# Optimization experiments

Measured on AMD Instinct MI355X. Metric: run time of the kernel, lower is better.

## Reference

```python
import jax, jax.numpy as jnp
import numpy as np


def setup_inputs() -> dict:
    key = jax.random.key(0)
    ks = jax.random.split(key, 12)
    B, C, H, W = 8, 256, 64, 64
    inter = C // 8
    s = 0.05  # weight scale keeps q.k logits in a stable softmax range
    f32 = jnp.float32
    x = jax.random.normal(ks[0], (B, C, H, W), f32)
    Wq = jax.random.normal(ks[1], (inter, C), f32) * s
    bq = jnp.zeros((inter,), f32)
    Wk = jax.random.normal(ks[2], (inter, C), f32) * s
    bk = jnp.zeros((inter,), f32)
    Wv = jax.random.normal(ks[3], (C, C), f32) * s
    bv = jnp.zeros((C,), f32)
    gamma = jnp.full((1,), 0.5, f32)  # learnable residual scale (init 0 in torch; 0.5 exercises the path)
    Wg1 = jax.random.normal(ks[4], (inter, C), f32) * s
    bg1 = jnp.zeros((inter,), f32)
    Wg2 = jax.random.normal(ks[5], (C, inter), f32) * s
    bg2 = jnp.zeros((C,), f32)
    return {"x": x, "Wq": Wq, "bq": bq, "Wk": Wk, "bk": bk, "Wv": Wv, "bv": bv,
            "gamma": gamma, "Wg1": Wg1, "bg1": bg1, "Wg2": Wg2, "bg2": bg2}


def reference(x, Wq, bq, Wk, bk, Wv, bv, gamma, Wg1, bg1, Wg2, bg2):
    B, C, H, W = x.shape
    N = H * W
    xf = x.reshape(B, C, N)  # [B,C,N]
    # 1x1 convs == per-pixel linear projections
    q = jnp.einsum('oc,bcn->bon', Wq, xf) + bq[None, :, None]  # [B,inter,N]
    k = jnp.einsum('oc,bcn->bon', Wk, xf) + bk[None, :, None]  # [B,inter,N]
    v = jnp.einsum('oc,bcn->bon', Wv, xf) + bv[None, :, None]  # [B,C,N]
    # attention[b,n,m] = softmax_m( q[b,:,n] . k[b,:,m] )
    attn = jax.nn.softmax(jnp.einsum('bin,bim->bnm', q, k), axis=-1)  # [B,N,N]
    # out[b,c,n] = sum_m v[b,c,m] * attn[b,n,m]
    out = jnp.einsum('bcm,bnm->bcn', v, attn)  # [B,C,N]
    out = gamma[0] * out + xf
    # gated global pooling branch: GAP -> 1x1 conv -> ReLU -> 1x1 conv -> Sigmoid
    gp = xf.mean(axis=-1)  # [B,C]
    h = jax.nn.relu(jnp.einsum('oc,bc->bo', Wg1, gp) + bg1)  # [B,inter]
    ga = jax.nn.sigmoid(jnp.einsum('co,bo->bc', Wg2, h) + bg2)  # [B,C]
    out = out * ga[:, :, None] + out
    return out.reshape(B, C, H, W)
```

## Files before the change

### kernel.cpp

```cpp
#include <hip/hip_runtime.h>

typedef unsigned short u16;
typedef unsigned int   u32;
typedef short s16x4 __attribute__((ext_vector_type(4)));
typedef u16 u16x4 __attribute__((ext_vector_type(4)));
typedef u16 u16x8 __attribute__((ext_vector_type(8)));
typedef __bf16 bf16x8 __attribute__((ext_vector_type(8)));
typedef float f32x4 __attribute__((ext_vector_type(4)));

#define NB 8
#define NC 256
#define NI 32
#define NN 4096
#define LOG2E 1.4426950408889634f
#define POFF 64.0f

#define OW_Q   0
#define OB_Q   8192
#define OW_K   8224
#define OB_K   16416
#define OW_V   16448
#define OB_V   81984
#define OGAM   82240
#define OW_G1  82248
#define OB_G1  90440
#define OW_G2  90472
#define OB_G2  98664
#define WTOT   98920

__device__ __forceinline__ float bf2f(u16 v) {
    u32 u = ((u32)v) << 16;
    return __builtin_bit_cast(float, u);
}
__device__ __forceinline__ u16 f2bf(float f) {
    u32 u = __builtin_bit_cast(u32, f);
    u32 lsb = (u >> 16) & 1u;
    u += 0x7fffu + lsb;
    return (u16)(u >> 16);
}
__device__ __forceinline__ bool is_f32_mode(const void* graw) {
    return ((const u16*)graw)[0] == 0;
}

__global__ __launch_bounds__(256) void convert_kernel(
    const void* x,  const void* Wq, const void* bq, const void* Wk, const void* bk,
    const void* Wv, const void* bv, const void* gamma, const void* Wg1, const void* bg1,
    const void* Wg2, const void* bg2, float* __restrict__ xf, float* __restrict__ wbuf,
    u16* __restrict__ wbf, float* __restrict__ gp)
{
    bool f32m = is_f32_mode(gamma);
    int blk = blockIdx.x, t = threadIdx.x;
    if (blk < 2048) {
        int base = blk * 4096 + t * 16;
        float s = 0.f;
        if (f32m) {
            const float* xs = (const float*)x;
#pragma unroll
            for (int k = 0; k < 4; ++k) {
                f32x4 a = *(const f32x4*)(xs + base + k * 4);
                s += (a[0] + a[1]) + (a[2] + a[3]);
            }
        } else {
            const u16* xs = (const u16*)x;
#pragma unroll
            for (int k = 0; k < 2; ++k) {
                u16x8 a = *(const u16x8*)(xs + base + k * 8);
                f32x4 lo, hi;
#pragma unroll
                for (int j = 0; j < 4; ++j) { lo[j] = bf2f(a[j]); hi[j] = bf2f(a[4 + j]); }
                *(f32x4*)(xf + base + k * 8)     = lo;
                *(f32x4*)(xf + base + k * 8 + 4) = hi;
                s += (lo[0]+lo[1])+(lo[2]+lo[3]) + (hi[0]+hi[1])+(hi[2]+hi[3]);
            }
        }
#pragma unroll
        for (int off = 1; off <= 32; off <<= 1) s += __shfl_xor(s, off, 64);
        __shared__ float ws[4];
        if ((t & 63) == 0) ws[t >> 6] = s;
        __syncthreads();
        if (t == 0) gp[blk] = (ws[0] + ws[1] + ws[2] + ws[3]) * (1.0f / NN);
        return;
    }
    if (blk < 2080) {
        int tid = (blk - 2048) * 256 + t;
        const int off[12] = {OW_Q, OB_Q, OW_K, OB_K, OW_V, OB_V, OGAM, OW_G1, OB_G1, OW_G2, OB_G2, WTOT};
        const int len[11] = {8192, 32, 8192, 32, 65536, 256, 1, 8192, 32, 8192, 256};
        const void* srcs[11] = {Wq, bq, Wk, bk, Wv, bv, gamma, Wg1, bg1, Wg2, bg2};
        for (int w = tid; w < WTOT; w += 32 * 256) {
            int seg = 0;
#pragma unroll
            for (int i = 1; i < 11; ++i) if (w >= off[i]) seg = i;
            int idx = w - off[seg];
            float val = 0.f;
            if (idx < len[seg])
                val = f32m ? ((const float*)srcs[seg])[idx] : bf2f(((const u16*)srcs[seg])[idx]);
            wbuf[w] = val;
        }
        return;
    }
    int tid = (blk - 2080) * 256 + t;
    for (int w = tid; w < 320 * 256; w += 10 * 256) {
        int row = w >> 8, c = w & 255;
        const void* src; int idx; float scale = 1.f;
        if (row < 32)      { src = Wq; idx = row * 256 + c; scale = LOG2E; }
        else if (row < 64) { src = Wk; idx = (row - 32) * 256 + c; }
        else               { src = Wv; idx = (row - 64) * 256 + c; }
        float val = f32m ? ((const float*)src)[idx] : bf2f(((const u16*)src)[idx]);
        wbf[w] = f2bf(val * scale);
    }
}

__global__ __launch_bounds__(256) void proj_kernel(
    const void* xr, const float* __restrict__ xf, const void* graw,
    const float* __restrict__ wbuf, const u16* __restrict__ wbf,
    u16* __restrict__ qt, u16* __restrict__ kt, u16* __restrict__ v)
{
    __shared__ __attribute__((aligned(16))) u16 xs[64][264];

    const float* X = is_f32_mode(graw) ? (const float*)xr : xf;

    int t    = threadIdx.x;
    int lane = t & 63;
    int wave = t >> 6;
    int b    = blockIdx.x >> 6;
    int m0   = (blockIdx.x & 63) << 6;
    int l15  = lane & 15;
    int quad = lane >> 4;

    {
        const float* xb = X + (size_t)b * NC * NN + m0 + lane;
        int c0 = wave * 64;
#pragma unroll
        for (int ci = 0; ci < 64; ci += 4) {
            int c = c0 + ci;
            float a0 = xb[(size_t)(c    ) * NN];
            float a1 = xb[(size_t)(c + 1) * NN];
            float a2 = xb[(size_t)(c + 2) * NN];
            float a3 = xb[(size_t)(c + 3) * NN];
            u16x4 p4 = { f2bf(a0), f2bf(a1), f2bf(a2), f2bf(a3) };
            *(u16x4*)&xs[lane][c] = p4;
        }
    }
    __syncthreads();

    const f32x4 zero4 = {};
    f32x4 acc[5][4];
#pragma unroll
    for (int i = 0; i < 5; ++i)
#pragma unroll
        for (int mt = 0; mt < 4; ++mt) acc[i][mt] = zero4;

    int obase = wave * 80;
    const u16* wb = wbf + (size_t)(obase + l15) * 256 + quad * 8;

    bf16x8 af[5];
#pragma unroll
    for (int i = 0; i < 5; ++i)
        af[i] = *(const bf16x8*)(wb + (size_t)(i * 16) * 256);

#pragma unroll
    for (int kc = 0; kc < 8; ++kc) {
        bf16x8 afn[5], bfr[4];
        if (kc < 7) {
#pragma unroll
            for (int i = 0; i < 5; ++i)
                afn[i] = *(const bf16x8*)(wb + (size_t)(i * 16) * 256 + (kc + 1) * 32);
        }
#pragma unroll
        for (int mt = 0; mt < 4; ++mt)
            bfr[mt] = *(const bf16x8*)&xs[mt * 16 + l15][kc * 32 + quad * 8];
#pragma unroll
        for (int i = 0; i < 5; ++i)
#pragma unroll
            for (int mt = 0; mt < 4; ++mt)
                acc[i][mt] = __builtin_amdgcn_mfma_f32_16x16x32_bf16(af[i], bfr[mt], acc[i][mt], 0, 0, 0);
        if (kc < 7) {
#pragma unroll
            for (int i = 0; i < 5; ++i) af[i] = afn[i];
        }
    }

    __syncthreads();

    if (wave == 0) {
#pragma unroll
        for (int i = 0; i < 4; ++i) {
#pragma unroll
            for (int mt = 0; mt < 4; ++mt) {
                u16x4 tmp;
#pragma unroll
                for (int r = 0; r < 4; ++r) {
                    int o = i * 16 + quad * 4 + r;
                    float bias = (o < 32) ? LOG2E * wbuf[OB_Q + o] : wbuf[OB_K + o - 32];
                    tmp[r] = f2bf(acc[i][mt][r] + bias);
                }
                *(u16x4*)&xs[mt * 16 + l15][i * 16 + quad * 4] = tmp;
            }
        }
        int m = m0 + lane;
        u16* qrow = qt + (size_t)(b * NN + m) * NI;
        u16* krow = kt + (size_t)(b * NN + m) * NI;
#pragma unroll
        for (int j = 0; j < 4; ++j) *(u16x8*)(qrow + j * 8) = *(const u16x8*)&xs[lane][j * 8];
#pragma unroll
        for (int j = 0; j < 4; ++j) *(u16x8*)(krow + j * 8) = *(const u16x8*)&xs[lane][32 + j * 8];
#pragma unroll
        for (int mt = 0; mt < 4; ++mt) {
#pragma unroll
            for (int r = 0; r < 4; ++r) {
                int c = quad * 4 + r;
                v[(size_t)(b * NC + c) * NN + m0 + mt * 16 + l15] = f2bf(acc[4][mt][r] + wbuf[OB_V + c]);
            }
        }
    } else {
#pragma unroll
        for (int i = 0; i < 5; ++i) {
#pragma unroll
            for (int mt = 0; mt < 4; ++mt) {
#pragma unroll
                for (int r = 0; r < 4; ++r) {
                    int c = wave * 80 + i * 16 + quad * 4 + r - 64;
                    v[(size_t)(b * NC + c) * NN + m0 + mt * 16 + l15] = f2bf(acc[i][mt][r] + wbuf[OB_V + c]);
                }
            }
        }
    }
}

__global__ __launch_bounds__(256) void gate_kernel(
    const float* __restrict__ gp, const float* __restrict__ wbuf, float* __restrict__ gmul)
{
    int b = blockIdx.x;
    int t = threadIdx.x;
    __shared__ float gps[NC];
    __shared__ float hs[NI];
    gps[t] = gp[b * NC + t];
    __syncthreads();
    if (t < NI) {
        float a = wbuf[OB_G1 + t];
        for (int c = 0; c < NC; ++c) a += wbuf[OW_G1 + t * NC + c] * gps[c];
        hs[t] = a > 0.f ? a : 0.f;
    }
    __syncthreads();
    float a = wbuf[OB_G2 + t];
#pragma unroll
    for (int i = 0; i < NI; ++i) a += wbuf[OW_G2 + t * NI + i] * hs[i];
    float sig = 1.f / (1.f + __expf(-a));
    gmul[b * NC + t] = 1.f + sig;
}

__global__ __launch_bounds__(512, 4) void flash_kernel(
    const u16* __restrict__ qt, const u16* __restrict__ kt, const u16* __restrict__ v,
    const void* xr, const float* __restrict__ xf, const void* graw,
    const float* __restrict__ wbuf, const float* __restrict__ gmul, void* outp)
{
    __shared__ __attribute__((aligned(16))) u16 vs[2][NC][48];

    bool f32m = is_f32_mode(graw);
    const float* X = f32m ? (const float*)xr : xf;

    int t    = threadIdx.x;
    int lane = t & 63;
    int wave = t >> 6;
    int b    = blockIdx.x >> 6;
    int nblk = (blockIdx.x & 63) << 6;
    int n0   = nblk + (wave >> 2) * 32;
    int c0   = (wave & 3) * 64;
    int l15  = lane & 15;
    int quad = lane >> 4;

    const f32x4 zero4 = {};

    bf16x8 qf[2];
#pragma unroll
    for (int n16 = 0; n16 < 2; ++n16)
        qf[n16] = *(const bf16x8*)(qt + (size_t)(b * NN + n0 + n16 * 16 + l15) * NI + quad * 8);

    f32x4 acc[2][4];
#pragma unroll
    for (int n16 = 0; n16 < 2; ++n16)
#pragma unroll
        for (int ct = 0; ct < 4; ++ct) acc[n16][ct] = zero4;
    float psum[2] = {0.f, 0.f};

    int sc = t >> 2;
    int sm = (t & 3) * 8;
    const u16* vb0 = v + (size_t)(b * NC + sc) * NN + sm;
    const u16* vb1 = v + (size_t)(b * NC + sc + 128) * NN + sm;
    const u16* ktb = kt + (size_t)(b * NN + l15) * NI + quad * 8;

    u16x8 vr0 = *(const u16x8*)vb0;
    u16x8 vr1 = *(const u16x8*)vb1;
    *(u16x8*)&vs[0][sc][sm]       = vr0;
    *(u16x8*)&vs[0][sc + 128][sm] = vr1;
    bf16x8 ktf[2];
#pragma unroll
    for (int mt = 0; mt < 2; ++mt)
        ktf[mt] = *(const bf16x8*)(ktb + (size_t)(mt * 16) * NI);
    __syncthreads();

    for (int it = 0; it < NN / 32; ++it) {
        int cur  = it & 1;
        bool more = (it < NN / 32 - 1);
        int mnxt = it * 32 + 32;

        if (more) {
            vr0 = *(const u16x8*)(vb0 + mnxt);
            vr1 = *(const u16x8*)(vb1 + mnxt);
        }

        f32x4 sf[2][2];
#pragma unroll
        for (int mt = 0; mt < 2; ++mt)
#pragma unroll
            for (int n16 = 0; n16 < 2; ++n16)
                sf[n16][mt] = __builtin_amdgcn_mfma_f32_16x16x32_bf16(ktf[mt], qf[n16], zero4, 0, 0, 0);

        if (more) {
#pragma unroll
            for (int mt = 0; mt < 2; ++mt)
                ktf[mt] = *(const bf16x8*)(ktb + (size_t)(mnxt + mt * 16) * NI);
        }

        s16x4 pfr[2][2];
#pragma unroll
        for (int n16 = 0; n16 < 2; ++n16)
#pragma unroll
            for (int mt = 0; mt < 2; ++mt) {
                float p0 = __builtin_amdgcn_exp2f(sf[n16][mt][0] - POFF);
                float p1 = __builtin_amdgcn_exp2f(sf[n16][mt][1] - POFF);
                float p2 = __builtin_amdgcn_exp2f(sf[n16][mt][2] - POFF);
                float p3 = __builtin_amdgcn_exp2f(sf[n16][mt][3] - POFF);
                psum[n16] += (p0 + p1) + (p2 + p3);
                pfr[n16][mt] = s16x4{ (short)f2bf(p0), (short)f2bf(p1),
                                      (short)f2bf(p2), (short)f2bf(p3) };
            }

#pragma unroll
        for (int mt = 0; mt < 2; ++mt) {
            int mb = mt * 16 + quad * 4;
#pragma unroll
            for (int ct = 0; ct < 4; ++ct) {
                s16x4 va = *(const s16x4*)&vs[cur][c0 + ct * 16 + l15][mb];
#pragma unroll
                for (int n16 = 0; n16 < 2; ++n16)
                    acc[n16][ct] = __builtin_amdgcn_mfma_f32_16x16x16bf16_1k(va, pfr[n16][mt], acc[n16][ct], 0, 0, 0);
            }
        }

        if (more) {
            *(u16x8*)&vs[cur ^ 1][sc][sm]       = vr0;
            *(u16x8*)&vs[cur ^ 1][sc + 128][sm] = vr1;
        }
        __syncthreads();
    }

    float inv[2];
#pragma unroll
    for (int n16 = 0; n16 < 2; ++n16) {
        float s = psum[n16];
        s += __shfl_xor(s, 16, 64);
        s += __shfl_xor(s, 32, 64);
        inv[n16] = 1.f / s;
    }
    float gam = wbuf[OGAM];

#pragma unroll
    for (int n16 = 0; n16 < 2; ++n16) {
        int n = n0 + n16 * 16 + l15;
#pragma unroll
        for (int ct = 0; ct < 4; ++ct) {
            int cb = c0 + ct * 16 + quad * 4;
            f32x4 gm4 = *(const f32x4*)&gmul[b * NC + cb];
#pragma unroll
            for (int r = 0; r < 4; ++r) {
                size_t off = (size_t)(b * NC + cb + r) * NN + n;
                float val = (gam * acc[n16][ct][r] * inv[n16] + X[off]) * gm4[r];
                if (f32m) ((float*)outp)[off] = val;
                else      ((u16*)outp)[off]  = f2bf(val);
            }
        }
    }
}

extern "C" void kernel_launch(void* const* d_in, const int* in_sizes, int n_in,
                              void* d_out, int out_size, void* d_ws, size_t ws_size,
                              hipStream_t stream)
{
    const void* x     = d_in[0];
    const void* Wq    = d_in[1];
    const void* bq    = d_in[2];
    const void* Wk    = d_in[3];
    const void* bk    = d_in[4];
    const void* Wv    = d_in[5];
    const void* bvp   = d_in[6];
    const void* gamma = d_in[7];
    const void* Wg1   = d_in[8];
    const void* bg1   = d_in[9];
    const void* Wg2   = d_in[10];
    const void* bg2   = d_in[11];

    char* ws = (char*)d_ws;
    float* xf   = (float*)ws;
    float* wbuf = (float*)(ws + 33554432);
    u16*   qt   = (u16*)  (ws + 33951744);
    u16*   kt   = (u16*)  (ws + 36048896);
    u16*   v    = (u16*)  (ws + 38146048);
    float* gp   = (float*)(ws + 54923264);
    float* gmul = (float*)(ws + 54931456);
    u16*   wbf  = (u16*)  (ws + 54939648);

    convert_kernel<<<2090, 256, 0, stream>>>(x, Wq, bq, Wk, bk, Wv, bvp, gamma,
                                             Wg1, bg1, Wg2, bg2, xf, wbuf, wbf, gp);
    proj_kernel<<<NB * 64, 256, 0, stream>>>(x, xf, gamma, wbuf, wbf, qt, kt, v);
    gate_kernel<<<NB, 256, 0, stream>>>(gp, wbuf, gmul);
    flash_kernel<<<NB * 64, 512, 0, stream>>>(qt, kt, v, x, xf, gamma, wbuf, gmul, d_out);
}
```

Baseline: 321.6 us.

## Drop LDS staging of V, read V fragments directly from global memory

Removes the double-buffered shared-memory tile for V and the per-iteration block barrier. Each wave now loads its V MFMA operands straight from global memory (relying on cache) and processes 64 keys per outer step with K prefetch. It also swaps the round-to-nearest bf16 conversion of probabilities for a truncating byte-permute pack. The trade is more global/L2 traffic and latency exposure per wave in exchange for no LDS or sync overhead, plus slightly less accurate bf16 rounding.

```diff
diff --git a/kernel.cpp b/kernel.cpp
--- a/kernel.cpp
+++ b/kernel.cpp
@@ -5,6 +5,7 @@
 typedef short s16x4 __attribute__((ext_vector_type(4)));
 typedef u16 u16x4 __attribute__((ext_vector_type(4)));
 typedef u16 u16x8 __attribute__((ext_vector_type(8)));
+typedef u32 u32x2 __attribute__((ext_vector_type(2)));
 typedef __bf16 bf16x8 __attribute__((ext_vector_type(8)));
 typedef float f32x4 __attribute__((ext_vector_type(4)));
 
@@ -37,6 +38,10 @@
     u32 lsb = (u >> 16) & 1u;
     u += 0x7fffu + lsb;
     return (u16)(u >> 16);
+}
+__device__ __forceinline__ u32 pack_trunc(float f0, float f1) {
+    return __builtin_amdgcn_perm(__builtin_bit_cast(u32, f1),
+                                 __builtin_bit_cast(u32, f0), 0x07060302u);
 }
 __device__ __forceinline__ bool is_f32_mode(const void* graw) {
     return ((const u16*)graw)[0] == 0;
@@ -254,8 +259,6 @@
     const void* xr, const float* __restrict__ xf, const void* graw,
     const float* __restrict__ wbuf, const float* __restrict__ gmul, void* outp)
 {
-    __shared__ __attribute__((aligned(16))) u16 vs[2][NC][48];
-
     bool f32m = is_f32_mode(graw);
     const float* X = f32m ? (const float*)xr : xf;
 
@@ -283,76 +286,63 @@
         for (int ct = 0; ct < 4; ++ct) acc[n16][ct] = zero4;
     float psum[2] = {0.f, 0.f};
 
-    int sc = t >> 2;
-    int sm = (t & 3) * 8;
-    const u16* vb0 = v + (size_t)(b * NC + sc) * NN + sm;
-    const u16* vb1 = v + (size_t)(b * NC + sc + 128) * NN + sm;
     const u16* ktb = kt + (size_t)(b * NN + l15) * NI + quad * 8;
-
-    u16x8 vr0 = *(const u16x8*)vb0;
-    u16x8 vr1 = *(const u16x8*)vb1;
-    *(u16x8*)&vs[0][sc][sm]       = vr0;
-    *(u16x8*)&vs[0][sc + 128][sm] = vr1;
-    bf16x8 ktf[2];
-#pragma unroll
-    for (int mt = 0; mt < 2; ++mt)
+    const u16* vfb = v + (size_t)(b * NC + c0 + l15) * NN + quad * 4;
+
+    bf16x8 ktf[4];
+#pragma unroll
+    for (int mt = 0; mt < 4; ++mt)
         ktf[mt] = *(const bf16x8*)(ktb + (size_t)(mt * 16) * NI);
-    __syncthreads();
-
-    for (int it = 0; it < NN / 32; ++it) {
-        int cur  = it & 1;
-        bool more = (it < NN / 32 - 1);
-        int mnxt = it * 32 + 32;
-
-        if (more) {
-            vr0 = *(const u16x8*)(vb0 + mnxt);
-            vr1 = *(const u16x8*)(vb1 + mnxt);
-        }
-
-        f32x4 sf[2][2];
-#pragma unroll
-        for (int mt = 0; mt < 2; ++mt)
+
+    for (int m0 = 0; m0 < NN; m0 += 64) {
+        bool more = (m0 + 64 < NN);
+#pragma unroll
+        for (int half = 0; half < 2; ++half) {
+            f32x4 sf[2][2];
+#pragma unroll
+            for (int mh = 0; mh < 2; ++mh)
+#pragma unroll
+                for (int n16 = 0; n16 < 2; ++n16)
+                    sf[n16][mh] = __builtin_amdgcn_mfma_f32_16x16x32_bf16(
+                        ktf[half * 2 + mh], qf[n16], zero4, 0, 0, 0);
+
+            if (half == 1) {
+                if (more) {
+#pragma unroll
+                    for (int mt = 0; mt < 4; ++mt)
+                        ktf[mt] = *(const bf16x8*)(ktb + (size_t)(m0 + 64 + mt * 16) * NI);
+                }
+            }
+
+            s16x4 pfr[2][2];
 #pragma unroll
             for (int n16 = 0; n16 < 2; ++n16)
-                sf[n16][mt] = __builtin_amdgcn_mfma_f32_16x16x32_bf16(ktf[mt], qf[n16], zero4, 0, 0, 0);
-
-        if (more) {
-#pragma unroll
-            for (int mt = 0; mt < 2; ++mt)
-                ktf[mt] = *(const bf16x8*)(ktb + (size_t)(mnxt + mt * 16) * NI);
-        }
-
-        s16x4 pfr[2][2];
-#pragma unroll
-        for (int n16 = 0; n16 < 2; ++n16)
-#pragma unroll
-            for (int mt = 0; mt < 2; ++mt) {
-                float p0 = __builtin_amdgcn_exp2f(sf[n16][mt][0] - POFF);
-                float p1 = __builtin_amdgcn_exp2f(sf[n16][mt][1] - POFF);
-                float p2 = __builtin_amdgcn_exp2f(sf[n16][mt][2] - POFF);
-                float p3 = __builtin_amdgcn_exp2f(sf[n16][mt][3] - POFF);
-                psum[n16] += (p0 + p1) + (p2 + p3);
-                pfr[n16][mt] = s16x4{ (short)f2bf(p0), (short)f2bf(p1),
-                                      (short)f2bf(p2), (short)f2bf(p3) };
-            }
-
-#pragma unroll
-        for (int mt = 0; mt < 2; ++mt) {
-            int mb = mt * 16 + quad * 4;
-#pragma unroll
-            for (int ct = 0; ct < 4; ++ct) {
-                s16x4 va = *(const s16x4*)&vs[cur][c0 + ct * 16 + l15][mb];
-#pragma unroll
-                for (int n16 = 0; n16 < 2; ++n16)
-                    acc[n16][ct] = __builtin_amdgcn_mfma_f32_16x16x16bf16_1k(va, pfr[n16][mt], acc[n16][ct], 0, 0, 0);
-            }
-        }
-
-        if (more) {
-            *(u16x8*)&vs[cur ^ 1][sc][sm]       = vr0;
-            *(u16x8*)&vs[cur ^ 1][sc + 128][sm] = vr1;
-        }
-        __syncthreads();
+#pragma unroll
+                for (int mh = 0; mh < 2; ++mh) {
+                    float p0 = __builtin_amdgcn_exp2f(sf[n16][mh][0] - POFF);
+                    float p1 = __builtin_amdgcn_exp2f(sf[n16][mh][1] - POFF);
+                    float p2 = __builtin_amdgcn_exp2f(sf[n16][mh][2] - POFF);
+                    float p3 = __builtin_amdgcn_exp2f(sf[n16][mh][3] - POFF);
+                    psum[n16] += (p0 + p1) + (p2 + p3);
+                    u32x2 w = { pack_trunc(p0, p1), pack_trunc(p2, p3) };
+                    pfr[n16][mh] = __builtin_bit_cast(s16x4, w);
+                }
+
+#pragma unroll
+            for (int mh = 0; mh < 2; ++mh) {
+                int mcol = m0 + (half * 2 + mh) * 16;
+                s16x4 va[4];
+#pragma unroll
+                for (int ct = 0; ct < 4; ++ct)
+                    va[ct] = *(const s16x4*)(vfb + (size_t)(ct * 16) * NN + mcol);
+#pragma unroll
+                for (int ct = 0; ct < 4; ++ct)
+#pragma unroll
+                    for (int n16 = 0; n16 < 2; ++n16)
+                        acc[n16][ct] = __builtin_amdgcn_mfma_f32_16x16x16bf16_1k(
+                            va[ct], pfr[n16][mh], acc[n16][ct], 0, 0, 0);
+            }
+        }
     }
 
     float inv[2];
```

Result: slower. 646.6 us (+101.1%).
